# Kernel optimization log

Measured on AMD Instinct MI355X. Metric: run time of the kernel, lower is better.

The kernel has to match this reference:

```python
import jax, jax.numpy as jnp
import numpy as np


def setup_inputs() -> dict:
    key = jax.random.key(0)
    ks = jax.random.split(key, 6)
    B, N, S, D, A = 32, 12, 512, 256, 96
    return {
        "value": jax.random.normal(ks[0], (B, N, S, D), dtype=jnp.float32),
        "emb": jax.random.normal(ks[1], (N, S, A), dtype=jnp.float32),
        "Wqk": jax.random.normal(ks[2], (A, D), dtype=jnp.float32) * (A ** -0.5),
        "bqk": jax.random.normal(ks[3], (D,), dtype=jnp.float32) * 0.02,
        "Wv": jax.random.normal(ks[4], (D, D), dtype=jnp.float32) * (D ** -0.5),
        "bv": jax.random.normal(ks[5], (D,), dtype=jnp.float32) * 0.02,
    }


def reference(value, emb, Wqk, bqk, Wv, bv):
    # qk: [n, s, d] -- query and key share the same projection FC_Q_K
    qk = emb @ Wqk + bqk
    v = value @ Wv + bv                      # [b, n, s, d]
    q = jax.nn.softmax(qk, axis=-1)          # softmax over d (last dim of query)
    k = jax.nn.softmax(qk.swapaxes(-1, -2), axis=-1)  # [n, d, s], softmax over s
    # key @ value: [n, d, s] x [b, n, s, e] -> [b, n, d, e] (broadcast over b)
    kv = jnp.einsum('nds,bnse->bnde', k, v)
    # query @ kv: [n, s, d] x [b, n, d, e] -> [b, n, s, e]
    out = jnp.einsum('nsd,bnde->bnse', q, kv)
    return out
```

## Files before the change

### kernel.cpp

```cpp
#include <hip/hip_runtime.h>
#include <hip/hip_bf16.h>

#define B_ 32
#define N_ 12
#define S_ 512
#define D_ 256
#define A_ 96

typedef __attribute__((ext_vector_type(8))) short short8;
typedef __attribute__((ext_vector_type(4))) float float4v;

static __device__ __forceinline__ ushort f2bf(float f) {
  union { float f; unsigned u; } a;
  a.f = f;
  return (ushort)((a.u + 0x7FFFu + ((a.u >> 16) & 1u)) >> 16);
}

static __device__ __forceinline__ void gload16(const ushort* g, ushort* l) {
  __builtin_amdgcn_global_load_lds(
      (const __attribute__((address_space(1))) unsigned int*)g,
      (__attribute__((address_space(3))) unsigned int*)l, 16, 0, 0);
}

__global__ __launch_bounds__(256) void k_qk_softmax_q(
    const float* __restrict__ emb, const float* __restrict__ Wqk,
    const float* __restrict__ bqk, float* __restrict__ qk,
    ushort* __restrict__ qb) {
  const int blk = blockIdx.x;
  const int tid = threadIdx.x;
  const int d = tid;
  const int wv = tid >> 6, lane = tid & 63;
  __shared__ float seT[A_][8];
  __shared__ float redm[8][4], reds[8][4];
  const float* ebase = emb + (size_t)blk * 8 * A_;
  for (int k = tid; k < 8 * A_; k += 256) {
    int r = k / A_, a = k - r * A_;
    seT[a][r] = ebase[k];
  }
  __syncthreads();
  float bq = bqk[d];
  float acc[8];
#pragma unroll
  for (int r = 0; r < 8; ++r) acc[r] = bq;
#pragma unroll 8
  for (int a = 0; a < A_; ++a) {
    float w = Wqk[a * D_ + d];
    float4 lo = *(const float4*)(&seT[a][0]);
    float4 hi = *(const float4*)(&seT[a][4]);
    acc[0] = fmaf(lo.x, w, acc[0]);
    acc[1] = fmaf(lo.y, w, acc[1]);
    acc[2] = fmaf(lo.z, w, acc[2]);
    acc[3] = fmaf(lo.w, w, acc[3]);
    acc[4] = fmaf(hi.x, w, acc[4]);
    acc[5] = fmaf(hi.y, w, acc[5]);
    acc[6] = fmaf(hi.z, w, acc[6]);
    acc[7] = fmaf(hi.w, w, acc[7]);
  }
  const size_t obase = (size_t)blk * 8 * D_ + d;
#pragma unroll
  for (int r = 0; r < 8; ++r) qk[obase + r * D_] = acc[r];
  float m[8];
#pragma unroll
  for (int r = 0; r < 8; ++r) {
    m[r] = acc[r];
    for (int off = 32; off; off >>= 1) m[r] = fmaxf(m[r], __shfl_xor(m[r], off));
  }
  if (lane == 0) {
#pragma unroll
    for (int r = 0; r < 8; ++r) redm[r][wv] = m[r];
  }
  __syncthreads();
  float e[8], s[8];
#pragma unroll
  for (int r = 0; r < 8; ++r) {
    float mm = fmaxf(fmaxf(redm[r][0], redm[r][1]),
                     fmaxf(redm[r][2], redm[r][3]));
    e[r] = __expf(acc[r] - mm);
    s[r] = e[r];
    for (int off = 32; off; off >>= 1) s[r] += __shfl_xor(s[r], off);
  }
  if (lane == 0) {
#pragma unroll
    for (int r = 0; r < 8; ++r) reds[r][wv] = s[r];
  }
  __syncthreads();
#pragma unroll
  for (int r = 0; r < 8; ++r) {
    float sum = reds[r][0] + reds[r][1] + reds[r][2] + reds[r][3];
    qb[obase + r * D_] = f2bf(e[r] / sum);
  }
}

__global__ __launch_bounds__(256) void k_softmax_kT(
    const float* __restrict__ qk, ushort* __restrict__ kTb) {
  const int dc = blockIdx.x * 4;
  const int n = blockIdx.y;
  const int tid = threadIdx.x;
  __shared__ float t[4][514];
  const float* base = qk + (size_t)n * S_ * D_ + dc;
#pragma unroll
  for (int it = 0; it < 2; ++it) {
    int s = it * 256 + tid;
    float4 v = *(const float4*)(base + (size_t)s * D_);
    t[0][s] = v.x;
    t[1][s] = v.y;
    t[2][s] = v.z;
    t[3][s] = v.w;
  }
  __syncthreads();
  const int d = tid >> 6, sg = tid & 63;
  float vv[8];
  float m = -1e30f;
#pragma unroll
  for (int k = 0; k < 8; ++k) {
    vv[k] = t[d][sg + 64 * k];
    m = fmaxf(m, vv[k]);
  }
  for (int off = 32; off; off >>= 1) m = fmaxf(m, __shfl_xor(m, off));
  float sum = 0.0f;
#pragma unroll
  for (int k = 0; k < 8; ++k) {
    vv[k] = __expf(vv[k] - m);
    sum += vv[k];
  }
  for (int off = 32; off; off >>= 1) sum += __shfl_xor(sum, off);
  float inv = 1.0f / sum;
  const size_t ob = ((size_t)n * D_ + dc + d) * S_;
#pragma unroll
  for (int k = 0; k < 8; ++k) kTb[ob + sg + 64 * k] = f2bf(vv[k] * inv);
}

__global__ __launch_bounds__(256) void k_wvt(const float* __restrict__ Wv,
                                             ushort* __restrict__ WvT) {
  int c = blockIdx.x, e = threadIdx.x;
  WvT[c * D_ + e] = f2bf(Wv[e * D_ + c]);
}

__global__ __launch_bounds__(512) void k_kv0(
    const ushort* __restrict__ kTb, const float* __restrict__ value,
    ushort* __restrict__ kv0) {
  const int f = blockIdx.x;
  const int wk = (f & 7) * 192 + (f >> 3);
  const int eq = wk & 3;
  const int bz = wk >> 2;
  const int n = bz % N_;
  const int tid = threadIdx.x;
  const int l = tid & 63, w = tid >> 6;
  const int lane16 = l & 15, quad = l >> 4;

  __shared__ ushort ldsV[2][64 * 72];

  const int se = tid & 63;
  const int sch = tid >> 6;
  const int schs = (sch ^ ((se >> 3) & 7)) << 3;
  const float* vbase = value + (size_t)bz * S_ * D_ + eq * 64 + se;
  const ushort* kTbase = kTb + (size_t)n * D_ * S_ + (w * 32) * S_;

  float4v acc[4][2];
#pragma unroll
  for (int i = 0; i < 4; ++i)
#pragma unroll
    for (int j = 0; j < 2; ++j) acc[i][j] = (float4v)0.0f;

  union Pack { ushort u[8]; uint4 v; };

  {
    float f0[8];
#pragma unroll
    for (int t = 0; t < 8; ++t) f0[t] = vbase[(size_t)(sch * 8 + t) * D_];
    Pack pk;
#pragma unroll
    for (int t = 0; t < 8; ++t) pk.u[t] = f2bf(f0[t]);
    *(uint4*)(&ldsV[0][se * 72 + schs]) = pk.v;
  }

  int p = 0;
  for (int sc = 0; sc < S_; sc += 64) {
    __syncthreads();
    float fs[8];
    const bool more = (sc + 64 < S_);
    if (more) {
#pragma unroll
      for (int t = 0; t < 8; ++t)
        fs[t] = vbase[(size_t)(sc + 64 + sch * 8 + t) * D_];
    }
#pragma unroll
    for (int kc = 0; kc < 64; kc += 32) {
      const int ko = kc + quad * 8;
      const int chr = ko >> 3;
      short8 a[4], b[2];
#pragma unroll
      for (int i = 0; i < 4; ++i) {
        int er = i * 16 + lane16;
        a[i] = *(const short8*)(
            &ldsV[p][er * 72 + ((chr ^ ((er >> 3) & 7)) << 3)]);
      }
#pragma unroll
      for (int j = 0; j < 2; ++j)
        b[j] = *(const short8*)(kTbase + (j * 16 + lane16) * S_ + sc + ko);
#pragma unroll
      for (int i = 0; i < 4; ++i)
#pragma unroll
        for (int j = 0; j < 2; ++j)
          acc[i][j] = __builtin_amdgcn_mfma_f32_16x16x32_bf16(a[i], b[j],
                                                              acc[i][j], 0, 0, 0);
    }
    if (more) {
      Pack pk;
#pragma unroll
      for (int t = 0; t < 8; ++t) pk.u[t] = f2bf(fs[t]);
      *(uint4*)(&ldsV[p ^ 1][se * 72 + schs]) = pk.v;
    }
    p ^= 1;
  }
  ushort* obase = kv0 + (size_t)bz * D_ * D_;
#pragma unroll
  for (int i = 0; i < 4; ++i) {
#pragma unroll
    for (int j = 0; j < 2; ++j) {
      int d = w * 32 + j * 16 + lane16;
      int e0 = eq * 64 + i * 16 + quad * 4;
      ushort4 pk;
      pk.x = f2bf(acc[i][j][0]);
      pk.y = f2bf(acc[i][j][1]);
      pk.z = f2bf(acc[i][j][2]);
      pk.w = f2bf(acc[i][j][3]);
      *(ushort4*)(obase + d * D_ + e0) = pk;
    }
  }
}

__global__ __launch_bounds__(256) void k_kvw_inplace(
    ushort* kv0, const ushort* __restrict__ WvT,
    const float* __restrict__ bv) {
  const int qd = blockIdx.x;
  const int bz = blockIdx.y;
  const int tid = threadIdx.x;
  const int l = tid & 63, w = tid >> 6;
  const int lane16 = l & 15, quad = l >> 4;
  const int srow = l >> 3, chp = l & 7;

  __shared__ ushort ldsA[64 * 64];
  __shared__ ushort ldsB[256 * 64];

  float4v acc[4][4];
#pragma unroll
  for (int i = 0; i < 4; ++i)
#pragma unroll
    for (int j = 0; j < 4; ++j) acc[i][j] = (float4v)0.0f;

  ushort* base = kv0 + (size_t)bz * (D_ * D_) + qd * (64 * D_);

  for (int ec = 0; ec < D_; ec += 64) {
    __syncthreads();
#pragma unroll
    for (int i = 0; i < 2; ++i) {
      int r = w * 16 + i * 8 + srow;
      gload16(base + (size_t)r * D_ + ec + ((chp ^ (r & 7)) << 3),
              &ldsA[(w * 16 + i * 8) * 64]);
    }
#pragma unroll
    for (int i = 0; i < 8; ++i) {
      int r = w * 64 + i * 8 + srow;
      gload16(WvT + (size_t)r * D_ + ec + ((chp ^ (r & 7)) << 3),
              &ldsB[(w * 64 + i * 8) * 64]);
    }
    __syncthreads();
#pragma unroll
    for (int kc = 0; kc < 64; kc += 32) {
      int ko = kc + quad * 8;
      int chr = ko >> 3;
      short8 a[4], b[4];
#pragma unroll
      for (int i = 0; i < 4; ++i) {
        int rr = i * 16 + lane16;
        a[i] = *(const short8*)(&ldsA[rr * 64 + ((chr ^ (rr & 7)) << 3)]);
      }
#pragma unroll
      for (int j = 0; j < 4; ++j) {
        int rc = w * 64 + j * 16 + lane16;
        b[j] = *(const short8*)(&ldsB[rc * 64 + ((chr ^ (rc & 7)) << 3)]);
      }
#pragma unroll
      for (int i = 0; i < 4; ++i)
#pragma unroll
        for (int j = 0; j < 4; ++j)
          acc[i][j] = __builtin_amdgcn_mfma_f32_16x16x32_bf16(a[i], b[j],
                                                              acc[i][j], 0, 0, 0);
    }
  }
#pragma unroll
  for (int i = 0; i < 4; ++i) {
#pragma unroll
    for (int j = 0; j < 4; ++j) {
      int c = w * 64 + j * 16 + lane16;
      int d0 = i * 16 + quad * 4;
      float bvc = bv[c];
      ushort4 p;
      p.x = f2bf(acc[i][j][0] + bvc);
      p.y = f2bf(acc[i][j][1] + bvc);
      p.z = f2bf(acc[i][j][2] + bvc);
      p.w = f2bf(acc[i][j][3] + bvc);
      *(ushort4*)(base + c * 64 + d0) = p;
    }
  }
}

__global__ __launch_bounds__(256) void k_out(
    const ushort* __restrict__ qb, const ushort* __restrict__ kvw,
    float* __restrict__ out) {
  const int f = blockIdx.x;
  const int wk = (f & 7) * 384 + (f >> 3);
  const int bx = wk & 3;
  const int by = (wk >> 2) & 1;
  const int bz = wk >> 3;
  const int n = bz % N_;
  const int tid = threadIdx.x;
  const int l = tid & 63, w = tid >> 6;
  const int wm = w & 1, wn = w >> 1;
  const int lane16 = l & 15, quad = l >> 4;
  const int srow = l >> 3, chp = l & 7;

  __shared__ ushort ldsA[128 * 64];
  __shared__ ushort ldsB[128 * 64];

  float4v acc[4][4];
#pragma unroll
  for (int i = 0; i < 4; ++i)
#pragma unroll
    for (int j = 0; j < 4; ++j) acc[i][j] = (float4v)0.0f;

  const ushort* abase = qb + (size_t)n * S_ * D_ + bx * 128 * D_;
  const ushort* bbase = kvw + (size_t)bz * D_ * D_;

  for (int dc = 0; dc < D_; dc += 64) {
    __syncthreads();
#pragma unroll
    for (int i = 0; i < 4; ++i) {
      int r = w * 32 + i * 8 + srow;
      gload16(abase + (size_t)r * D_ + dc + ((chp ^ (r & 7)) << 3),
              &ldsA[(w * 32 + i * 8) * 64]);
    }
#pragma unroll
    for (int i = 0; i < 4; ++i) {
      int r = w * 32 + i * 8 + srow;
      gload16(bbase + (dc >> 6) * 16384 + (by * 128 + r) * 64 +
                  ((chp ^ (r & 7)) << 3),
              &ldsB[(w * 32 + i * 8) * 64]);
    }
    __syncthreads();
#pragma unroll
    for (int kc = 0; kc < 64; kc += 32) {
      int ko = kc + quad * 8;
      int chr = ko >> 3;
      short8 a[4], b[4];
#pragma unroll
      for (int i = 0; i < 4; ++i) {
        int rr = wm * 64 + i * 16 + lane16;
        a[i] = *(const short8*)(&ldsA[rr * 64 + ((chr ^ (rr & 7)) << 3)]);
      }
#pragma unroll
      for (int j = 0; j < 4; ++j) {
        int rc = wn * 64 + j * 16 + lane16;
        b[j] = *(const short8*)(&ldsB[rc * 64 + ((chr ^ (rc & 7)) << 3)]);
      }
#pragma unroll
      for (int i = 0; i < 4; ++i)
#pragma unroll
        for (int j = 0; j < 4; ++j)
          acc[i][j] = __builtin_amdgcn_mfma_f32_16x16x32_bf16(a[i], b[j],
                                                              acc[i][j], 0, 0, 0);
    }
  }
  float* obase = out + (size_t)bz * S_ * D_;
#pragma unroll
  for (int i = 0; i < 4; ++i) {
#pragma unroll
    for (int j = 0; j < 4; ++j) {
      int s0 = bx * 128 + wm * 64 + i * 16 + quad * 4;
      int c = by * 128 + wn * 64 + j * 16 + lane16;
#pragma unroll
      for (int r = 0; r < 4; ++r)
        obase[(s0 + r) * D_ + c] = acc[i][j][r];
    }
  }
}

extern "C" void kernel_launch(void* const* d_in, const int* in_sizes, int n_in,
                              void* d_out, int out_size, void* d_ws,
                              size_t ws_size, hipStream_t stream) {
  const float* value = (const float*)d_in[0];
  const float* emb   = (const float*)d_in[1];
  const float* Wqk   = (const float*)d_in[2];
  const float* bqk   = (const float*)d_in[3];
  const float* Wv    = (const float*)d_in[4];
  const float* bv    = (const float*)d_in[5];
  float* out = (float*)d_out;

  char* ws = (char*)d_ws;
  float*  qk  = (float*)ws;
  ushort* qb  = (ushort*)(ws + 6291456);
  ushort* kTb = (ushort*)(ws + 9437184);
  ushort* kv0 = (ushort*)(ws + 12582912);
  ushort* WvT = (ushort*)(ws + 62914560);

  k_qk_softmax_q<<<dim3(N_ * S_ / 8), 256, 0, stream>>>(emb, Wqk, bqk, qk, qb);
  k_softmax_kT<<<dim3(64, N_), 256, 0, stream>>>(qk, kTb);
  k_wvt<<<dim3(D_), 256, 0, stream>>>(Wv, WvT);
  k_kv0<<<dim3(4 * B_ * N_), 512, 0, stream>>>(kTb, value, kv0);
  k_kvw_inplace<<<dim3(4, B_ * N_), 256, 0, stream>>>(kv0, WvT, bv);
  k_out<<<dim3(4 * 2 * B_ * N_), 256, 0, stream>>>(qb, kv0, out);
}
```

Measured before the change: 458.5 us.

## Fuse key-value product and value projection into one kernel with LDS-parked intermediate

Merges the k@V kernel and the in-place Wv projection kernel into a single kernel. Each block now computes a 64-row slice of d against all 256 e columns, parks the bf16 result in shared memory, then multiplies it by WvT and adds the bias. This removes the global round-trip of the kv0 intermediate and one launch. In exchange, each block now reads the full value tile for its batch-head (four times redundant across blocks), the value loads are no longer double-buffered, and shared memory use is large (about 70KB), which may limit occupancy.

```diff
diff --git a/kernel.cpp b/kernel.cpp
--- a/kernel.cpp
+++ b/kernel.cpp
@@ -136,54 +136,52 @@
   WvT[c * D_ + e] = f2bf(Wv[e * D_ + c]);
 }
 
-__global__ __launch_bounds__(512) void k_kv0(
+__global__ __launch_bounds__(512, 4) void k_kv_fused2(
     const ushort* __restrict__ kTb, const float* __restrict__ value,
-    ushort* __restrict__ kv0) {
+    const ushort* __restrict__ WvT, const float* __restrict__ bv,
+    ushort* __restrict__ kvw) {
   const int f = blockIdx.x;
   const int wk = (f & 7) * 192 + (f >> 3);
-  const int eq = wk & 3;
+  const int qd = wk & 3;
   const int bz = wk >> 2;
   const int n = bz % N_;
   const int tid = threadIdx.x;
   const int l = tid & 63, w = tid >> 6;
   const int lane16 = l & 15, quad = l >> 4;
 
-  __shared__ ushort ldsV[2][64 * 72];
-
-  const int se = tid & 63;
-  const int sch = tid >> 6;
-  const int schs = (sch ^ ((se >> 3) & 7)) << 3;
-  const float* vbase = value + (size_t)bz * S_ * D_ + eq * 64 + se;
-  const ushort* kTbase = kTb + (size_t)n * D_ * S_ + (w * 32) * S_;
-
+  __shared__ ushort smem[35328];
+  ushort* park = smem;
+  ushort* ldsV = smem + 16896;
+  ushort* ldsW = smem + 16896;
+
+  const int wd = w & 1, we = w >> 1;
   float4v acc[4][2];
 #pragma unroll
   for (int i = 0; i < 4; ++i)
 #pragma unroll
     for (int j = 0; j < 2; ++j) acc[i][j] = (float4v)0.0f;
 
+  const int sE = tid & 255;
+  const int sH = tid >> 8;
+  const float* vbase = value + (size_t)bz * S_ * D_ + sE;
+  const ushort* kTbase = kTb + (size_t)n * D_ * S_ + (qd * 64 + wd * 32) * S_;
   union Pack { ushort u[8]; uint4 v; };
 
-  {
-    float f0[8];
-#pragma unroll
-    for (int t = 0; t < 8; ++t) f0[t] = vbase[(size_t)(sch * 8 + t) * D_];
-    Pack pk;
-#pragma unroll
-    for (int t = 0; t < 8; ++t) pk.u[t] = f2bf(f0[t]);
-    *(uint4*)(&ldsV[0][se * 72 + schs]) = pk.v;
-  }
-
-  int p = 0;
   for (int sc = 0; sc < S_; sc += 64) {
     __syncthreads();
-    float fs[8];
-    const bool more = (sc + 64 < S_);
-    if (more) {
+#pragma unroll
+    for (int cc = 0; cc < 4; ++cc) {
+      float fv[8];
 #pragma unroll
       for (int t = 0; t < 8; ++t)
-        fs[t] = vbase[(size_t)(sc + 64 + sch * 8 + t) * D_];
-    }
+        fv[t] = vbase[(size_t)(sc + sH * 32 + cc * 8 + t) * D_];
+      Pack pk;
+#pragma unroll
+      for (int t = 0; t < 8; ++t) pk.u[t] = f2bf(fv[t]);
+      int ch = sH * 4 + cc;
+      *(uint4*)(&ldsV[sE * 72 + ((ch ^ ((sE >> 3) & 7)) << 3)]) = pk.v;
+    }
+    __syncthreads();
 #pragma unroll
     for (int kc = 0; kc < 64; kc += 32) {
       const int ko = kc + quad * 8;
@@ -191,9 +189,9 @@
       short8 a[4], b[2];
 #pragma unroll
       for (int i = 0; i < 4; ++i) {
-        int er = i * 16 + lane16;
+        int er = we * 64 + i * 16 + lane16;
         a[i] = *(const short8*)(
-            &ldsV[p][er * 72 + ((chr ^ ((er >> 3) & 7)) << 3)]);
+            &ldsV[er * 72 + ((chr ^ ((er >> 3) & 7)) << 3)]);
       }
 #pragma unroll
       for (int j = 0; j < 2; ++j)
@@ -205,103 +203,71 @@
           acc[i][j] = __builtin_amdgcn_mfma_f32_16x16x32_bf16(a[i], b[j],
                                                               acc[i][j], 0, 0, 0);
     }
-    if (more) {
-      Pack pk;
-#pragma unroll
-      for (int t = 0; t < 8; ++t) pk.u[t] = f2bf(fs[t]);
-      *(uint4*)(&ldsV[p ^ 1][se * 72 + schs]) = pk.v;
-    }
-    p ^= 1;
-  }
-  ushort* obase = kv0 + (size_t)bz * D_ * D_;
+  }
 #pragma unroll
   for (int i = 0; i < 4; ++i) {
 #pragma unroll
     for (int j = 0; j < 2; ++j) {
-      int d = w * 32 + j * 16 + lane16;
-      int e0 = eq * 64 + i * 16 + quad * 4;
-      ushort4 pk;
-      pk.x = f2bf(acc[i][j][0]);
-      pk.y = f2bf(acc[i][j][1]);
-      pk.z = f2bf(acc[i][j][2]);
-      pk.w = f2bf(acc[i][j][3]);
-      *(ushort4*)(obase + d * D_ + e0) = pk;
-    }
-  }
-}
-
-__global__ __launch_bounds__(256) void k_kvw_inplace(
-    ushort* kv0, const ushort* __restrict__ WvT,
-    const float* __restrict__ bv) {
-  const int qd = blockIdx.x;
-  const int bz = blockIdx.y;
-  const int tid = threadIdx.x;
-  const int l = tid & 63, w = tid >> 6;
-  const int lane16 = l & 15, quad = l >> 4;
-  const int srow = l >> 3, chp = l & 7;
-
-  __shared__ ushort ldsA[64 * 64];
-  __shared__ ushort ldsB[256 * 64];
-
-  float4v acc[4][4];
-#pragma unroll
-  for (int i = 0; i < 4; ++i)
-#pragma unroll
-    for (int j = 0; j < 4; ++j) acc[i][j] = (float4v)0.0f;
-
-  ushort* base = kv0 + (size_t)bz * (D_ * D_) + qd * (64 * D_);
+      int dl = wd * 32 + j * 16 + lane16;
+      int e0 = we * 64 + i * 16 + quad * 4;
+      ushort4 p;
+      p.x = f2bf(acc[i][j][0]);
+      p.y = f2bf(acc[i][j][1]);
+      p.z = f2bf(acc[i][j][2]);
+      p.w = f2bf(acc[i][j][3]);
+      *(ushort4*)(&park[dl * 264 + e0]) = p;
+    }
+  }
+
+  const int wd2 = w & 1, wc = w >> 1;
+  float4v acc2[2][4];
+#pragma unroll
+  for (int i = 0; i < 2; ++i)
+#pragma unroll
+    for (int j = 0; j < 4; ++j) acc2[i][j] = (float4v)0.0f;
 
   for (int ec = 0; ec < D_; ec += 64) {
     __syncthreads();
 #pragma unroll
-    for (int i = 0; i < 2; ++i) {
-      int r = w * 16 + i * 8 + srow;
-      gload16(base + (size_t)r * D_ + ec + ((chp ^ (r & 7)) << 3),
-              &ldsA[(w * 16 + i * 8) * 64]);
-    }
-#pragma unroll
-    for (int i = 0; i < 8; ++i) {
-      int r = w * 64 + i * 8 + srow;
-      gload16(WvT + (size_t)r * D_ + ec + ((chp ^ (r & 7)) << 3),
-              &ldsB[(w * 64 + i * 8) * 64]);
+    for (int it = 0; it < 4; ++it) {
+      int id = it * 512 + tid;
+      int r = id >> 3, cc = (id & 7) * 8;
+      *(uint4*)(&ldsW[r * 72 + cc]) = *(const uint4*)(WvT + r * D_ + ec + cc);
     }
     __syncthreads();
 #pragma unroll
     for (int kc = 0; kc < 64; kc += 32) {
-      int ko = kc + quad * 8;
-      int chr = ko >> 3;
-      short8 a[4], b[4];
-#pragma unroll
-      for (int i = 0; i < 4; ++i) {
-        int rr = i * 16 + lane16;
-        a[i] = *(const short8*)(&ldsA[rr * 64 + ((chr ^ (rr & 7)) << 3)]);
-      }
-#pragma unroll
-      for (int j = 0; j < 4; ++j) {
-        int rc = w * 64 + j * 16 + lane16;
-        b[j] = *(const short8*)(&ldsB[rc * 64 + ((chr ^ (rc & 7)) << 3)]);
-      }
-#pragma unroll
-      for (int i = 0; i < 4; ++i)
+      const int ko = kc + quad * 8;
+      short8 a[2], b[4];
+#pragma unroll
+      for (int i = 0; i < 2; ++i)
+        a[i] = *(const short8*)(
+            &park[(wd2 * 32 + i * 16 + lane16) * 264 + ec + ko]);
+#pragma unroll
+      for (int j = 0; j < 4; ++j)
+        b[j] = *(const short8*)(&ldsW[(wc * 64 + j * 16 + lane16) * 72 + ko]);
+#pragma unroll
+      for (int i = 0; i < 2; ++i)
 #pragma unroll
         for (int j = 0; j < 4; ++j)
-          acc[i][j] = __builtin_amdgcn_mfma_f32_16x16x32_bf16(a[i], b[j],
-                                                              acc[i][j], 0, 0, 0);
-    }
-  }
-#pragma unroll
-  for (int i = 0; i < 4; ++i) {
+          acc2[i][j] = __builtin_amdgcn_mfma_f32_16x16x32_bf16(a[i], b[j],
+                                                               acc2[i][j], 0, 0, 0);
+    }
+  }
+  ushort* obase = kvw + (size_t)bz * (D_ * D_) + qd * 16384;
+#pragma unroll
+  for (int i = 0; i < 2; ++i) {
 #pragma unroll
     for (int j = 0; j < 4; ++j) {
-      int c = w * 64 + j * 16 + lane16;
-      int d0 = i * 16 + quad * 4;
+      int c = wc * 64 + j * 16 + lane16;
+      int dl0 = wd2 * 32 + i * 16 + quad * 4;
       float bvc = bv[c];
       ushort4 p;
-      p.x = f2bf(acc[i][j][0] + bvc);
-      p.y = f2bf(acc[i][j][1] + bvc);
-      p.z = f2bf(acc[i][j][2] + bvc);
-      p.w = f2bf(acc[i][j][3] + bvc);
-      *(ushort4*)(base + c * 64 + d0) = p;
+      p.x = f2bf(acc2[i][j][0] + bvc);
+      p.y = f2bf(acc2[i][j][1] + bvc);
+      p.z = f2bf(acc2[i][j][2] + bvc);
+      p.w = f2bf(acc2[i][j][3] + bvc);
+      *(ushort4*)(obase + c * 64 + dl0) = p;
     }
   }
 }
@@ -401,13 +367,12 @@
   float*  qk  = (float*)ws;
   ushort* qb  = (ushort*)(ws + 6291456);
   ushort* kTb = (ushort*)(ws + 9437184);
-  ushort* kv0 = (ushort*)(ws + 12582912);
+  ushort* kvw = (ushort*)(ws + 12582912);
   ushort* WvT = (ushort*)(ws + 62914560);
 
   k_qk_softmax_q<<<dim3(N_ * S_ / 8), 256, 0, stream>>>(emb, Wqk, bqk, qk, qb);
   k_softmax_kT<<<dim3(64, N_), 256, 0, stream>>>(qk, kTb);
   k_wvt<<<dim3(D_), 256, 0, stream>>>(Wv, WvT);
-  k_kv0<<<dim3(4 * B_ * N_), 512, 0, stream>>>(kTb, value, kv0);
-  k_kvw_inplace<<<dim3(4, B_ * N_), 256, 0, stream>>>(kv0, WvT, bv);
-  k_out<<<dim3(4 * 2 * B_ * N_), 256, 0, stream>>>(qb, kv0, out);
-}
+  k_kv_fused2<<<dim3(4 * B_ * N_), 512, 0, stream>>>(kTb, value, WvT, bv, kvw);
+  k_out<<<dim3(4 * 2 * B_ * N_), 256, 0, stream>>>(qb, kvw, out);
+}
```

Result: slower. 474.5 us (+3.5%).
